# Kernel tuning notes

Measured on AMD Instinct MI355X. Metric: run time of the kernel, lower is better.

## Reference

```python
import jax, jax.numpy as jnp
import numpy as np

B, S, D, H = 32, 8192, 128, 256  # batch-of-MLPs, seq_len, emb_dim, hidden_dim
LN_EPS = 1e-5


def setup_inputs() -> dict:
    key = jax.random.key(0)
    k0, k1, k2, k3 = jax.random.split(key, 4)
    x = jax.random.normal(k0, (B, S, D), dtype=jnp.float32)
    # shared learned Q projection (torch Linear stores W as [out,in]; y = x @ W.T)
    Wq = jax.random.normal(k1, (D, D), dtype=jnp.float32) / np.float32(np.sqrt(D))
    # per-batch-index (non-shared) fast-weight MLP params
    W1 = jax.random.normal(k2, (B, D, H), dtype=jnp.float32) / np.float32(np.sqrt(D))
    b1 = jnp.zeros((B, H), dtype=jnp.float32)
    W2 = jax.random.normal(k3, (B, H, D), dtype=jnp.float32) / np.float32(np.sqrt(H))
    b2 = jnp.zeros((B, D), dtype=jnp.float32)
    gamma = jnp.ones((B, D), dtype=jnp.float32)
    beta = jnp.zeros((B, D), dtype=jnp.float32)
    return dict(x=x, Wq=Wq, W1=W1, b1=b1, W2=W2, b2=b2, gamma=gamma, beta=beta)


def reference(x, Wq, W1, b1, W2, b2, gamma, beta):
    # queries = silu(Q(x))
    q = jax.nn.silu(jnp.einsum('bsd,ed->bse', x, Wq))
    # torch F.normalize with default dim=1 -> L2-normalize over the sequence axis
    q = q / jnp.clip(jnp.linalg.norm(q, axis=1, keepdims=True), 1e-12)
    # ParallelMLPs: per-index MLP with distinct weights (grouped GEMM), + residual
    h = jax.nn.silu(jnp.einsum('bsd,bdh->bsh', q, W1) + b1[:, None, :])
    o = jnp.einsum('bsh,bhd->bsd', h, W2) + b2[:, None, :]
    mu = jnp.mean(o, axis=-1, keepdims=True)
    var = jnp.mean(jnp.square(o - mu), axis=-1, keepdims=True)
    ln = (o - mu) / jnp.sqrt(var + LN_EPS) * gamma[:, None, :] + beta[:, None, :]
    return ln + q
```

## Files before the change

kernel.cpp:

```cpp
#include <hip/hip_runtime.h>
#include <stdint.h>

#define B_ 32
#define S_ 8192
#define D_ 128
#define H_ 256

typedef __attribute__((ext_vector_type(4))) float f32x4;
typedef __attribute__((ext_vector_type(16))) float f32x16;
typedef __attribute__((ext_vector_type(8))) short bf16x8;
typedef __attribute__((ext_vector_type(4))) unsigned int u32x4;

__device__ __forceinline__ unsigned short f2bf(float f) {
    union { float f; unsigned int u; } v; v.f = f;
    unsigned int r = v.u + 0x7fffu + ((v.u >> 16) & 1u);
    return (unsigned short)(r >> 16);
}
__device__ __forceinline__ float bf2f(unsigned short u) {
    union { unsigned int u; float f; } v; v.u = ((unsigned int)u) << 16;
    return v.f;
}
__device__ __forceinline__ float silu_f(float v) {
    return v * __builtin_amdgcn_rcpf(1.0f + __expf(-v));
}
__device__ __forceinline__ unsigned int cvtpk(float lo, float hi) {
    unsigned int r;
    asm("v_cvt_pk_bf16_f32 %0, %1, %2" : "=v"(r) : "v"(lo), "v"(hi));
    return r;
}
__device__ __forceinline__ void plswap(unsigned int& a, unsigned int& b) {
    asm("v_permlane32_swap_b32 %0, %1" : "+v"(a), "+v"(b));
}
__device__ __forceinline__ void gl16(const void* g, void* l) {
    __builtin_amdgcn_global_load_lds(
        (const __attribute__((address_space(1))) unsigned int*)g,
        (__attribute__((address_space(3))) unsigned int*)l, 16, 0, 0);
}

__global__ void k_prep(const float* __restrict__ Wq, const float* __restrict__ W1,
                       const float* __restrict__ W2, const float* __restrict__ b1,
                       unsigned short* __restrict__ wq_bf,
                       unsigned short* __restrict__ w1s,
                       unsigned short* __restrict__ w2s,
                       float* __restrict__ b1r) {
    __shared__ __align__(16) unsigned short tile[8192];
    int t = threadIdx.x, blk = blockIdx.x;
    if (blk < 128) {
        int b = blk >> 2, hc = blk & 3;
#pragma unroll
        for (int i = 0; i < 8; i++) {
            int idx = t + i * 256;
            int d = idx >> 4, hj = idx & 15;
            f32x4 v = *(const f32x4*)(W1 + ((size_t)(b * D_ + d)) * H_ + hc * 64 + hj * 4);
#pragma unroll
            for (int u = 0; u < 4; u++) tile[(hj * 4 + u) * 128 + d] = f2bf(v[u]);
        }
        __syncthreads();
        char* img = (char*)w1s + (size_t)blk * 16384;
#pragma unroll
        for (int i = 0; i < 4; i++) {
            int c = t + i * 256;
            int n = c >> 9, kk = (c >> 6) & 7, l = c & 63;
            u32x4 v = *(const u32x4*)(tile + (n * 32 + (l & 31)) * 128 + kk * 16 + (l >> 5) * 8);
            *(u32x4*)(img + c * 16) = v;
        }
    } else if (blk < 256) {
        int a = blk - 128;
        int b = a >> 2, hc = a & 3;
#pragma unroll
        for (int i = 0; i < 8; i++) {
            int idx = t + i * 256;
            int h = idx >> 5, d4 = idx & 31;
            f32x4 v = *(const f32x4*)(W2 + ((size_t)(b * H_ + hc * 64 + h)) * D_ + d4 * 4);
#pragma unroll
            for (int u = 0; u < 4; u++) tile[(d4 * 4 + u) * 64 + h] = f2bf(v[u]);
        }
        __syncthreads();
        char* img = (char*)w2s + (size_t)a * 16384;
#pragma unroll
        for (int i = 0; i < 4; i++) {
            int c = t + i * 256;
            int dn = c >> 8, n = (c >> 7) & 1, kk2 = (c >> 6) & 1, l = c & 63;
            u32x4 v = *(const u32x4*)(tile + (dn * 32 + (l & 31)) * 64 + n * 32 + kk2 * 16 + (l >> 5) * 8);
            *(u32x4*)(img + c * 16) = v;
        }
    } else if (blk < 320) {
        int i = (blk - 256) * 256 + t;
        wq_bf[i] = f2bf(Wq[i]);
    } else {
        int idx = (blk - 320) * 256 + t;
        int b = idx >> 8, rem = idx & 255;
        int hc = rem >> 6, n = (rem >> 5) & 1, hi = (rem >> 4) & 1, r = rem & 15;
        int h = hc * 64 + n * 32 + (r & 3) + 8 * (r >> 2) + 4 * hi;
        b1r[idx] = b1[b * H_ + h];
    }
}

__global__ __launch_bounds__(256, 2) void k_qproj(
        const float* __restrict__ x, const unsigned short* __restrict__ wq_bf,
        unsigned short* __restrict__ q_img, float* __restrict__ part) {
    __shared__ __align__(16) unsigned short lds_a[128 * 128];
    __shared__ __align__(16) unsigned short lds_b[128 * 128];
    __shared__ float lds_ss[4][128];

    int tid = threadIdx.x;
    int lane = tid & 63, w = tid >> 6;
    int g = lane >> 4, c15 = lane & 15;
    int blk = blockIdx.x;
    int b = blk >> 6, st = blk & 63;
    size_t rowbase = (size_t)b * S_ + (size_t)st * 128;
    const float* xg = x + rowbase * D_;

    char* pA = (char*)lds_a;
    char* pB = (char*)lds_b;

#pragma unroll
    for (int i = 0; i < 8; i++) {
        int idx = tid + i * 256;
        int row = idx >> 4, cb = idx & 15;
        u32x4 v = *(const u32x4*)(wq_bf + row * 128 + cb * 8);
        *(u32x4*)(pB + row * 256 + (((unsigned)cb ^ (unsigned)(row & 7)) << 4)) = v;
    }
#pragma unroll
    for (int i = 0; i < 16; i++) {
        int idx = tid + i * 256;
        int row = idx >> 5, c4 = idx & 31;
        f32x4 v = *(const f32x4*)(xg + (size_t)row * 128 + c4 * 4);
        unsigned int lo = cvtpk(v[0], v[1]), hi2 = cvtpk(v[2], v[3]);
        *(unsigned long long*)(pA + row * 256 + ((c4 * 8) ^ ((row & 7) << 4))) =
            ((unsigned long long)hi2 << 32) | (unsigned long long)lo;
    }
    __syncthreads();

    f32x4 acc[2][8];
#pragma unroll
    for (int m = 0; m < 2; m++)
#pragma unroll
        for (int n = 0; n < 8; n++) acc[m][n] = (f32x4)0.0f;

#pragma unroll
    for (int kk = 0; kk < 4; kk++) {
        int kb = kk * 64 + (g << 4);
        bf16x8 a[2];
#pragma unroll
        for (int m = 0; m < 2; m++) {
            int row = (w << 5) + (m << 4) + c15;
            a[m] = *(const bf16x8*)(pA + row * 256 + (kb ^ ((row & 7) << 4)));
        }
#pragma unroll
        for (int n = 0; n < 8; n++) {
            int rowb = (n << 4) + c15;
            bf16x8 bb = *(const bf16x8*)(pB + rowb * 256 + (kb ^ ((rowb & 7) << 4)));
#pragma unroll
            for (int m = 0; m < 2; m++)
                acc[m][n] = __builtin_amdgcn_mfma_f32_16x16x32_bf16(a[m], bb, acc[m][n], 0, 0, 0);
        }
    }

    float ss[8];
#pragma unroll
    for (int n = 0; n < 8; n++) ss[n] = 0.0f;
#pragma unroll
    for (int m = 0; m < 2; m++)
#pragma unroll
        for (int n = 0; n < 8; n++)
#pragma unroll
            for (int r = 0; r < 4; r++) {
                float v = silu_f(acc[m][n][r]);
                acc[m][n][r] = v;
                ss[n] += v * v;
            }
#pragma unroll
    for (int n = 0; n < 8; n++) {
        float v = ss[n];
        v += __shfl_xor(v, 16, 64);
        v += __shfl_xor(v, 32, 64);
        if (lane < 16) lds_ss[w][(n << 4) + lane] = v;
    }
    __syncthreads();

#pragma unroll
    for (int m = 0; m < 2; m++)
#pragma unroll
        for (int n = 0; n < 8; n++)
#pragma unroll
            for (int r = 0; r < 4; r++) {
                int row = (w << 5) + (m << 4) + (g << 2) + r;
                int col = (n << 4) + c15;
                int byte = (row >> 5) * 8192 + (col >> 4) * 1024 +
                           ((row & 31) + ((col >> 3) & 1) * 32) * 16 + (col & 7) * 2;
                *(unsigned short*)(pA + byte) = f2bf(acc[m][n][r]);
            }
    __syncthreads();

    char* qo = (char*)q_img + ((size_t)(b * 256 + st * 4)) * 8192;
#pragma unroll
    for (int i = 0; i < 8; i++) {
        int off = tid * 16 + i * 4096;
        *(u32x4*)(qo + off) = *(const u32x4*)(pA + off);
    }
    if (tid < 128) {
        float s = lds_ss[0][tid] + lds_ss[1][tid] + lds_ss[2][tid] + lds_ss[3][tid];
        part[((size_t)b * 64 + st) * 128 + tid] = s;
    }
}

__global__ void k_scale(const float* __restrict__ part, float* __restrict__ scale) {
    int idx = blockIdx.x * 256 + threadIdx.x;
    int b = idx >> 7, e = idx & 127;
    const float* p = part + (size_t)b * 64 * 128 + e;
    float s = 0.0f;
    for (int t = 0; t < 64; t++) s += p[t * 128];
    scale[idx] = 1.0f / fmaxf(sqrtf(s), 1e-12f);
}

__global__ void k_wscale(unsigned short* __restrict__ w1s, const float* __restrict__ scale) {
    int blk = blockIdx.x;
    int b = blk >> 2;
    char* region = (char*)w1s + (size_t)blk * 16384;
    int t = threadIdx.x;
#pragma unroll
    for (int i = 0; i < 4; i++) {
        int c = t + i * 256;
        int kk = (c >> 6) & 7, l = c & 63;
        int d0 = kk * 16 + (l >> 5) * 8;
        u32x4 v = *(const u32x4*)(region + c * 16);
        const unsigned short* pv = (const unsigned short*)&v;
        const float* sc = scale + b * D_ + d0;
        u32x4 o;
#pragma unroll
        for (int j = 0; j < 4; j++)
            o[j] = cvtpk(bf2f(pv[2 * j]) * sc[2 * j], bf2f(pv[2 * j + 1]) * sc[2 * j + 1]);
        *(u32x4*)(region + c * 16) = o;
    }
}

__global__ __launch_bounds__(256, 2) void k_mlp(
        const unsigned short* __restrict__ q_img, const float* __restrict__ scale,
        const unsigned short* __restrict__ w1s, const unsigned short* __restrict__ w2s,
        const float* __restrict__ b1r, const float* __restrict__ b2,
        const float* __restrict__ gamma, const float* __restrict__ beta,
        float* __restrict__ out) {
    __shared__ __align__(16) char lds[32768];
    int tid = threadIdx.x;
    int lane = tid & 63, w = tid >> 6;
    int c31 = lane & 31, hi = lane >> 5;
    int blk = blockIdx.x;
    int b = blk >> 6, st = blk & 63;

    const char* w1b = (const char*)w1s + (size_t)(b * 4) * 16384;
    const char* w2b = (const char*)w2s + (size_t)(b * 4) * 16384;
    size_t grp = (size_t)(b * 256 + st * 4 + w);
    const char* qg = (const char*)q_img + grp * 8192;

#define STAGE(hcn) do {                                                        \
    _Pragma("unroll")                                                          \
    for (int i_ = 0; i_ < 4; i_++) {                                           \
        int off_ = w * 1024 + i_ * 4096;                                       \
        gl16(w1b + (hcn) * 16384 + off_ + lane * 16, lds + off_);              \
        gl16(w2b + (hcn) * 16384 + off_ + lane * 16, lds + 16384 + off_);      \
    } } while (0)

    STAGE(0);

    bf16x8 qf[8];
#pragma unroll
    for (int kk = 0; kk < 8; kk++)
        qf[kk] = *(const bf16x8*)(qg + kk * 1024 + lane * 16);

    f32x16 acco[4];
#pragma unroll
    for (int dn = 0; dn < 4; dn++)
#pragma unroll
        for (int e = 0; e < 16; e++) acco[dn][e] = 0.0f;

    __syncthreads();

#pragma unroll 1
    for (int hc = 0; hc < 4; hc++) {
        bf16x8 pa[2][2];
#pragma unroll
        for (int n = 0; n < 2; n++) {
            const float* b1p = b1r + ((b * 4 + hc) * 2 + n) * 32 + hi * 16;
            f32x16 acch;
#pragma unroll
            for (int jq = 0; jq < 4; jq++) {
                f32x4 bq = *(const f32x4*)(b1p + jq * 4);
#pragma unroll
                for (int e = 0; e < 4; e++) acch[jq * 4 + e] = bq[e];
            }
#pragma unroll
            for (int kk = 0; kk < 8; kk++) {
                bf16x8 wf = *(const bf16x8*)(lds + n * 8192 + kk * 1024 + lane * 16);
                acch = __builtin_amdgcn_mfma_f32_32x32x16_bf16(wf, qf[kk], acch, 0, 0, 0);
            }
            float sv[16];
#pragma unroll
            for (int r = 0; r < 16; r++) sv[r] = silu_f(acch[r]);
            unsigned int P[8];
#pragma unroll
            for (int p = 0; p < 8; p++) P[p] = cvtpk(sv[2 * p], sv[2 * p + 1]);
            plswap(P[0], P[2]); plswap(P[1], P[3]);
            plswap(P[4], P[6]); plswap(P[5], P[7]);
            union { unsigned int u[4]; bf16x8 v; } f0, f1;
            f0.u[0] = P[0]; f0.u[1] = P[1]; f0.u[2] = P[2]; f0.u[3] = P[3];
            f1.u[0] = P[4]; f1.u[1] = P[5]; f1.u[2] = P[6]; f1.u[3] = P[7];
            pa[n][0] = f0.v; pa[n][1] = f1.v;
        }

#pragma unroll
        for (int dn = 0; dn < 4; dn++)
#pragma unroll
            for (int n = 0; n < 2; n++)
#pragma unroll
                for (int kk2 = 0; kk2 < 2; kk2++) {
                    bf16x8 wf2 = *(const bf16x8*)(lds + 16384 + dn * 4096 +
                                                  n * 2048 + kk2 * 1024 + lane * 16);
                    acco[dn] = __builtin_amdgcn_mfma_f32_32x32x16_bf16(pa[n][kk2], wf2, acco[dn], 0, 0, 0);
                }

        if (hc < 3) {
            __syncthreads();
            STAGE(hc + 1);
            __syncthreads();
        }
    }
#undef STAGE

    __syncthreads();
    char* myq = (char*)lds + w * 8192;
#pragma unroll
    for (int kk = 0; kk < 8; kk++)
        *(bf16x8*)(myq + c31 * 256 + ((kk * 32 + hi * 16) ^ ((c31 & 7) << 4))) = qf[kk];

    float scv[4], gv[4], bev[4], b2v[4];
#pragma unroll
    for (int dn = 0; dn < 4; dn++) {
        int d = dn * 32 + c31;
        scv[dn] = scale[b * 128 + d];
        gv[dn]  = gamma[b * 128 + d];
        bev[dn] = beta[b * 128 + d];
        b2v[dn] = b2[b * 128 + d];
    }

    float* og = out + grp * 32 * 128;
#pragma unroll
    for (int r = 0; r < 16; r++) {
        float v0 = acco[0][r] + b2v[0], v1 = acco[1][r] + b2v[1];
        float v2 = acco[2][r] + b2v[2], v3 = acco[3][r] + b2v[3];
        float s1 = (v0 + v1) + (v2 + v3);
        float s2 = (v0 * v0 + v1 * v1) + (v2 * v2 + v3 * v3);
        s1 += __shfl_xor(s1, 1, 64);   s2 += __shfl_xor(s2, 1, 64);
        s1 += __shfl_xor(s1, 2, 64);   s2 += __shfl_xor(s2, 2, 64);
        s1 += __shfl_xor(s1, 4, 64);   s2 += __shfl_xor(s2, 4, 64);
        s1 += __shfl_xor(s1, 8, 64);   s2 += __shfl_xor(s2, 8, 64);
        s1 += __shfl_xor(s1, 16, 64);  s2 += __shfl_xor(s2, 16, 64);
        float mu = s1 * (1.0f / 128.0f);
        float var = s2 * (1.0f / 128.0f) - mu * mu;
        float rstd = rsqrtf(var + 1e-5f);
        int srow0 = (r & 3) + 8 * (r >> 2);
        int row = srow0 + 4 * hi;
        float vv[4] = {v0, v1, v2, v3};
#pragma unroll
        for (int dn = 0; dn < 4; dn++) {
            float qv = bf2f(*(const unsigned short*)(myq + row * 256 +
                        ((dn * 64 + c31 * 2) ^ ((row & 7) << 4)))) * scv[dn];
            float o = (vv[dn] - mu) * rstd * gv[dn] + bev[dn] + qv;
            og[(size_t)row * 128 + dn * 32 + c31] = o;
        }
    }
}

extern "C" void kernel_launch(void* const* d_in, const int* in_sizes, int n_in,
                              void* d_out, int out_size, void* d_ws, size_t ws_size,
                              hipStream_t stream) {
    (void)in_sizes; (void)n_in; (void)out_size; (void)ws_size;
    const float* x     = (const float*)d_in[0];
    const float* Wq    = (const float*)d_in[1];
    const float* W1    = (const float*)d_in[2];
    const float* b1    = (const float*)d_in[3];
    const float* W2    = (const float*)d_in[4];
    const float* b2    = (const float*)d_in[5];
    const float* gamma = (const float*)d_in[6];
    const float* beta  = (const float*)d_in[7];
    float* out = (float*)d_out;

    char* ws = (char*)d_ws;
    unsigned short* wq_bf = (unsigned short*)(ws);
    unsigned short* w1s   = (unsigned short*)(ws + 32768);
    unsigned short* w2s   = (unsigned short*)(ws + 2129920);
    float* part           = (float*)(ws + 4227072);
    float* scale          = (float*)(ws + 5275648);
    float* b1r            = (float*)(ws + 5292032);
    unsigned short* q_img = (unsigned short*)(ws + 5324800);

    hipLaunchKernelGGL(k_prep, dim3(352), dim3(256), 0, stream, Wq, W1, W2, b1, wq_bf, w1s, w2s, b1r);
    hipLaunchKernelGGL(k_qproj, dim3(2048), dim3(256), 0, stream, x, wq_bf, q_img, part);
    hipLaunchKernelGGL(k_scale, dim3(16), dim3(256), 0, stream, part, scale);
    hipLaunchKernelGGL(k_wscale, dim3(128), dim3(256), 0, stream, w1s, scale);
    hipLaunchKernelGGL(k_mlp, dim3(2048), dim3(256), 0, stream,
                       q_img, scale, w1s, w2s, b1r, b2, gamma, beta, out);
}
```

Baseline: 137.6 us.

## Read MLP weights directly from global memory instead of staging through LDS

Drops the LDS staging of W1/W2 chunks, along with the block-wide barriers around each stage, and has every wave load weight fragments straight from global (L2-cached) memory. The hidden loop is fully unrolled, the second GEMM is interleaved per n-half, and the q tile is written to LDS up front. Block indices are also remapped so that blocks sharing a batch's weights are spread across XCDs differently. The aim is to remove synchronization stalls, at the cost of more global/L2 traffic and load latency sitting on the MFMA chain, plus higher register pressure from the full unroll.

```diff
diff --git a/kernel.cpp b/kernel.cpp
--- a/kernel.cpp
+++ b/kernel.cpp
@@ -30,11 +30,6 @@
 }
 __device__ __forceinline__ void plswap(unsigned int& a, unsigned int& b) {
     asm("v_permlane32_swap_b32 %0, %1" : "+v"(a), "+v"(b));
-}
-__device__ __forceinline__ void gl16(const void* g, void* l) {
-    __builtin_amdgcn_global_load_lds(
-        (const __attribute__((address_space(1))) unsigned int*)g,
-        (__attribute__((address_space(3))) unsigned int*)l, 16, 0, 0);
 }
 
 __global__ void k_prep(const float* __restrict__ Wq, const float* __restrict__ W1,
@@ -246,39 +241,35 @@
     int lane = tid & 63, w = tid >> 6;
     int c31 = lane & 31, hi = lane >> 5;
     int blk = blockIdx.x;
-    int b = blk >> 6, st = blk & 63;
+    int k = blk & 7, j = blk >> 3;
+    int b = k * 4 + (j >> 6);
+    int st = j & 63;
 
     const char* w1b = (const char*)w1s + (size_t)(b * 4) * 16384;
     const char* w2b = (const char*)w2s + (size_t)(b * 4) * 16384;
     size_t grp = (size_t)(b * 256 + st * 4 + w);
     const char* qg = (const char*)q_img + grp * 8192;
 
-#define STAGE(hcn) do {                                                        \
-    _Pragma("unroll")                                                          \
-    for (int i_ = 0; i_ < 4; i_++) {                                           \
-        int off_ = w * 1024 + i_ * 4096;                                       \
-        gl16(w1b + (hcn) * 16384 + off_ + lane * 16, lds + off_);              \
-        gl16(w2b + (hcn) * 16384 + off_ + lane * 16, lds + 16384 + off_);      \
-    } } while (0)
-
-    STAGE(0);
-
     bf16x8 qf[8];
 #pragma unroll
     for (int kk = 0; kk < 8; kk++)
         qf[kk] = *(const bf16x8*)(qg + kk * 1024 + lane * 16);
 
+    char* myq = (char*)lds + w * 8192;
+#pragma unroll
+    for (int kk = 0; kk < 8; kk++)
+        *(bf16x8*)(myq + c31 * 256 + ((kk * 32 + hi * 16) ^ ((c31 & 7) << 4))) = qf[kk];
+
     f32x16 acco[4];
 #pragma unroll
     for (int dn = 0; dn < 4; dn++)
 #pragma unroll
         for (int e = 0; e < 16; e++) acco[dn][e] = 0.0f;
 
-    __syncthreads();
-
-#pragma unroll 1
+#pragma unroll
     for (int hc = 0; hc < 4; hc++) {
-        bf16x8 pa[2][2];
+        const char* w1h = w1b + hc * 16384;
+        const char* w2h = w2b + hc * 16384;
 #pragma unroll
         for (int n = 0; n < 2; n++) {
             const float* b1p = b1r + ((b * 4 + hc) * 2 + n) * 32 + hi * 16;
@@ -291,7 +282,7 @@
             }
 #pragma unroll
             for (int kk = 0; kk < 8; kk++) {
-                bf16x8 wf = *(const bf16x8*)(lds + n * 8192 + kk * 1024 + lane * 16);
+                bf16x8 wf = *(const bf16x8*)(w1h + n * 8192 + kk * 1024 + lane * 16);
                 acch = __builtin_amdgcn_mfma_f32_32x32x16_bf16(wf, qf[kk], acch, 0, 0, 0);
             }
             float sv[16];
@@ -305,33 +296,16 @@
             union { unsigned int u[4]; bf16x8 v; } f0, f1;
             f0.u[0] = P[0]; f0.u[1] = P[1]; f0.u[2] = P[2]; f0.u[3] = P[3];
             f1.u[0] = P[4]; f1.u[1] = P[5]; f1.u[2] = P[6]; f1.u[3] = P[7];
-            pa[n][0] = f0.v; pa[n][1] = f1.v;
-        }
-
-#pragma unroll
-        for (int dn = 0; dn < 4; dn++)
-#pragma unroll
-            for (int n = 0; n < 2; n++)
-#pragma unroll
-                for (int kk2 = 0; kk2 < 2; kk2++) {
-                    bf16x8 wf2 = *(const bf16x8*)(lds + 16384 + dn * 4096 +
-                                                  n * 2048 + kk2 * 1024 + lane * 16);
-                    acco[dn] = __builtin_amdgcn_mfma_f32_32x32x16_bf16(pa[n][kk2], wf2, acco[dn], 0, 0, 0);
-                }
-
-        if (hc < 3) {
-            __syncthreads();
-            STAGE(hc + 1);
-            __syncthreads();
-        }
-    }
-#undef STAGE
-
-    __syncthreads();
-    char* myq = (char*)lds + w * 8192;
-#pragma unroll
-    for (int kk = 0; kk < 8; kk++)
-        *(bf16x8*)(myq + c31 * 256 + ((kk * 32 + hi * 16) ^ ((c31 & 7) << 4))) = qf[kk];
+            bf16x8 pa0 = f0.v, pa1 = f1.v;
+#pragma unroll
+            for (int dn = 0; dn < 4; dn++) {
+                bf16x8 wf20 = *(const bf16x8*)(w2h + dn * 4096 + n * 2048 + lane * 16);
+                bf16x8 wf21 = *(const bf16x8*)(w2h + dn * 4096 + n * 2048 + 1024 + lane * 16);
+                acco[dn] = __builtin_amdgcn_mfma_f32_32x32x16_bf16(pa0, wf20, acco[dn], 0, 0, 0);
+                acco[dn] = __builtin_amdgcn_mfma_f32_32x32x16_bf16(pa1, wf21, acco[dn], 0, 0, 0);
+            }
+        }
+    }
 
     float scv[4], gv[4], bev[4], b2v[4];
 #pragma unroll
```

Measured after the change: 153.1 us. 1.11x slower.
